# Optimization experiments

Measured on AMD Instinct MI355X. Metric: run time of the kernel, lower is better.

Reference implementation:

```python
import jax, jax.numpy as jnp
import numpy as np

HIDDEN, HEADS, HDIM = 1024, 8, 64
B, S = 4, 8192
LN_EPS = 1e-6


def setup_inputs() -> dict:
    key = jax.random.key(0)
    ks = jax.random.split(key, 12)
    inner = HEADS * HDIM
    sd = HIDDEN ** -0.5
    return {
        "x": jax.random.normal(ks[0], (B, S, HIDDEN), jnp.float32),
        "Wq": jax.random.normal(ks[1], (HIDDEN, inner), jnp.float32) * sd,
        "bq": jnp.zeros((inner,), jnp.float32),
        "Wk": jax.random.normal(ks[2], (HIDDEN, inner), jnp.float32) * sd,
        "bk": jnp.zeros((inner,), jnp.float32),
        "Wv": jax.random.normal(ks[3], (HIDDEN, inner), jnp.float32) * sd,
        "bv": jnp.zeros((inner,), jnp.float32),
        "Wo": jax.random.normal(ks[4], (inner, HIDDEN), jnp.float32) * (inner ** -0.5),
        "bo": jnp.zeros((HIDDEN,), jnp.float32),
        "alpha": jnp.ones((HEADS, HDIM), jnp.float32),
        "aug_param": jax.random.normal(ks[5], (1, HEADS, HDIM), jnp.float32),
        "ln_scale": jnp.ones((HIDDEN,), jnp.float32),
        "ln_bias": jnp.zeros((HIDDEN,), jnp.float32),
    }


def reference(x, Wq, bq, Wk, bk, Wv, bv, Wo, bo, alpha, aug_param, ln_scale, ln_bias):
    b, s, _ = x.shape
    h, d = alpha.shape
    scale = d ** -0.5
    q = (x @ Wq + bq).reshape(b, s, h, d)
    k = (x @ Wk + bk).reshape(b, s, h, d)
    v = (x @ Wv + bv).reshape(b, s, h, d)
    decay = jax.nn.sigmoid(alpha)  # (h, d)

    def step(state, qkv):
        q_t, k_t, v_t = qkv  # each (b, h, d)
        attn = jax.nn.softmax(jnp.einsum('bhd,bhd->bh', q_t, k_t) * scale, axis=-1)
        new_state = decay * state + (1.0 - decay) * attn[..., None] * v_t
        return new_state, new_state

    qs = jnp.moveaxis(q, 1, 0)  # (s, b, h, d)
    ks_ = jnp.moveaxis(k, 1, 0)
    vs = jnp.moveaxis(v, 1, 0)
    init = jnp.zeros((b, h, d), x.dtype)
    _, states = jax.lax.scan(step, init, (qs, ks_, vs))
    states = jnp.moveaxis(states, 0, 1)  # (b, s, h, d)

    aug = jax.nn.sigmoid(q * aug_param)  # aug_param (1,h,d) broadcasts over (b,s,h,d)
    out = (q * states + aug).reshape(b, s, h * d)
    out = out @ Wo + bo
    mean = jnp.mean(out, axis=-1, keepdims=True)
    var = jnp.var(out, axis=-1, keepdims=True)
    return (out - mean) * jax.lax.rsqrt(var + LN_EPS) * ln_scale + ln_bias
```

## Files before the change

### kernel.cpp

```cpp
#include <hip/hip_runtime.h>
#include <hip/hip_bf16.h>


#define HIDDEN 1024
#define HEADS 8
#define HDIM 64
#define INNER 512
#define BATCH 4
#define SEQ 8192
#define ROWS (BATCH*SEQ)
#define NCHUNK 128
#define CHLEN 64

typedef unsigned short u16;
typedef unsigned int u32;
typedef __attribute__((ext_vector_type(8))) short bf16x8;
typedef __attribute__((ext_vector_type(4))) float f32x4;

__device__ __forceinline__ float b2f(u16 u) { return __uint_as_float(((u32)u) << 16); }
__device__ __forceinline__ u16 f2b(float f) {
  u32 u = __float_as_uint(f);
  u32 r = u + 0x7fffu + ((u >> 16) & 1u);
  return (u16)(r >> 16);
}
__device__ __forceinline__ u32 pack2(float a, float b) {
  return (u32)f2b(a) | ((u32)f2b(b) << 16);
}

#define GLOAD_LDS16(gp, lp)                                                  \
  __builtin_amdgcn_global_load_lds(                                          \
      (const __attribute__((address_space(1))) u32*)(gp),                    \
      (__attribute__((address_space(3))) u32*)(lp), 16, 0, 0)

__global__ __launch_bounds__(256) void prep_x(const float* __restrict__ x,
                                              u16* __restrict__ xb) {
  size_t i = ((size_t)blockIdx.x * 256 + threadIdx.x) * 8;
  float4 a = *(const float4*)(x + i);
  float4 b = *(const float4*)(x + i + 4);
  uint4 w = {pack2(a.x, a.y), pack2(a.z, a.w), pack2(b.x, b.y), pack2(b.z, b.w)};
  *(uint4*)(xb + i) = w;
}

__global__ __launch_bounds__(256) void prep_w(
    const float* __restrict__ Wq, const float* __restrict__ Wk,
    const float* __restrict__ Wv, const float* __restrict__ Wo,
    const float* __restrict__ bq, const float* __restrict__ bk,
    const float* __restrict__ bv,
    u16* __restrict__ Wt, u16* __restrict__ Wot, float* __restrict__ bcat) {
  const int WELEM = HIDDEN * INNER;
  int idx = blockIdx.x * 256 + threadIdx.x;
  if (idx < 3 * WELEM) {
    int z = idx / WELEM;
    int rem = idx - z * WELEM;
    int n = rem >> 10;
    int k = rem & 1023;
    const float* W = (z == 0) ? Wq : (z == 1) ? Wk : Wv;
    Wt[idx] = f2b(W[k * INNER + n]);
  } else {
    int rem = idx - 3 * WELEM;
    int n = rem >> 9;
    int k = rem & 511;
    Wot[rem] = f2b(Wo[k * HIDDEN + n]);
  }
  if (idx < 3 * INNER) {
    int z = idx >> 9;
    int n = idx & 511;
    bcat[idx] = (z == 0) ? bq[n] : (z == 1) ? bk[n] : bv[n];
  }
}

template <int K, bool OUT_F32, bool SPLIT3>
__global__ __launch_bounds__(512, 2) void gemm_ring(
    const u16* __restrict__ A, const u16* __restrict__ Bt,
    const float* __restrict__ bias,
    void* __restrict__ out0, void* __restrict__ out1, void* __restrict__ out2,
    int nTilesN) {
  constexpr int NT = K / 32;
  __shared__ u16 lds[4][16384];

  const int nwg = gridDim.x;
  const int chunk = nwg >> 3;
  const int bid = blockIdx.x;
  const int lin = (bid & 7) * chunk + (bid >> 3);
  const int nt = lin % nTilesN;
  const int mt = lin / nTilesN;
  const int m0 = mt * 256, n0 = nt * 256;
  const int N = nTilesN * 256;

  const int tid = threadIdx.x;
  const int lane = tid & 63;
  const int w = tid >> 6;
  const int wm = w >> 2;
  const int wn = w & 3;
  const int r16 = lane & 15, kq = lane >> 4;

  const int rt = tid >> 2;
  const int cg = (((tid & 3) ^ (rt & 3)) << 3);
  const u16* Ag = A + (size_t)(m0 + rt) * K + cg;
  const u16* Bg = Bt + (size_t)(n0 + rt) * K + cg;
  const int ldst = w * 512;

#define STAGE(slot, kt)                                                       \
  {                                                                           \
    const u16* ga = Ag + (size_t)(kt) * 32;                                   \
    const u16* gb = Bg + (size_t)(kt) * 32;                                   \
    GLOAD_LDS16(ga, &lds[slot][ldst]);                                        \
    GLOAD_LDS16(ga + (size_t)128 * K, &lds[slot][4096 + ldst]);               \
    GLOAD_LDS16(gb, &lds[slot][8192 + ldst]);                                 \
    GLOAD_LDS16(gb + (size_t)128 * K, &lds[slot][12288 + ldst]);              \
  }

  const int xr = (r16 & 3) << 3;
  const int aO = (wm * 128 + r16) * 32 + ((kq << 3) ^ xr);
  const int bO = 8192 + (wn * 64 + r16) * 32 + ((kq << 3) ^ xr);

  f32x4 acc[8][4] = {};

#define COMPUTE(slot)                                                          \
  {                                                                            \
    const u16* sl = &lds[slot][0];                                             \
    bf16x8 af[8], bfv[4];                                                      \
    _Pragma("unroll") for (int j = 0; j < 4; j++)                              \
        bfv[j] = *(const bf16x8*)&sl[bO + j * 512];                            \
    _Pragma("unroll") for (int i = 0; i < 8; i++)                              \
        af[i] = *(const bf16x8*)&sl[aO + i * 512];                             \
    _Pragma("unroll") for (int i = 0; i < 8; i++)                              \
        _Pragma("unroll") for (int j = 0; j < 4; j++)                          \
            acc[i][j] =                                                        \
        __builtin_amdgcn_mfma_f32_16x16x32_bf16(af[i], bfv[j], acc[i][j], 0, 0, 0); \
  }

#define SYNCB                                                                  \
  {                                                                            \
    __builtin_amdgcn_sched_barrier(0);                                         \
    __builtin_amdgcn_s_barrier();                                              \
    __builtin_amdgcn_sched_barrier(0);                                         \
  }

  STAGE(0, 0);
  STAGE(1, 1);
  STAGE(2, 2);

  for (int t = 0; t < NT - 3; ++t) {
    STAGE((t + 3) & 3, t + 3);
    asm volatile("s_waitcnt vmcnt(12)" ::: "memory");
    SYNCB;
    COMPUTE(t & 3);
    SYNCB;
  }
  asm volatile("s_waitcnt vmcnt(8)" ::: "memory");
  SYNCB;
  COMPUTE((NT - 3) & 3);
  SYNCB;
  asm volatile("s_waitcnt vmcnt(4)" ::: "memory");
  SYNCB;
  COMPUTE((NT - 2) & 3);
  SYNCB;
  asm volatile("s_waitcnt vmcnt(0)" ::: "memory");
  SYNCB;
  COMPUTE((NT - 1) & 3);
#undef STAGE
#undef COMPUTE
#undef SYNCB

  const int zsel = SPLIT3 ? ((n0 + wn * 64) >> 9) : 0;
  u16* ob16 = (u16*)((zsel == 0) ? out0 : (zsel == 1) ? out1 : out2);
#pragma unroll
  for (int j = 0; j < 4; j++) {
    int col = n0 + wn * 64 + j * 16 + r16;
    float bv = bias[col];
    int colm = SPLIT3 ? (col & 511) : col;
#pragma unroll
    for (int i = 0; i < 8; i++) {
#pragma unroll
      for (int q = 0; q < 4; q++) {
        int row = m0 + wm * 128 + i * 16 + kq * 4 + q;
        float v = acc[i][j][q] + bv;
        if (OUT_F32)
          ((float*)out0)[(size_t)row * N + col] = v;
        else
          ob16[(size_t)row * INNER + colm] = f2b(v);
      }
    }
  }
}

template <bool A_BF16, bool OUT_F32>
__global__ __launch_bounds__(256) void gemm128(
    const void* __restrict__ Aany, const u16* __restrict__ BtBase,
    const float* __restrict__ bias0, const float* __restrict__ bias1,
    const float* __restrict__ bias2,
    void* __restrict__ out0, void* __restrict__ out1, void* __restrict__ out2,
    int K) {
  __shared__ u16 As[128 * 32];
  __shared__ u16 Bs[128 * 32];
  const int N = gridDim.x * 128;
  const int z = blockIdx.z;
  const u16* Bt = BtBase + (size_t)z * N * K;
  const float* bias = (z == 0) ? bias0 : (z == 1) ? bias1 : bias2;
  void* Out = (z == 0) ? out0 : (z == 1) ? out1 : out2;
  const int tid = threadIdx.x;
  const int m0 = blockIdx.y * 128;
  const int n0 = blockIdx.x * 128;
  const int lane = tid & 63;
  const int wid = tid >> 6;
  const int wm = wid >> 1, wn = wid & 1;
  const int r16 = lane & 15, kq = lane >> 4;
  const int r = tid >> 1;
  const int half = tid & 1;
  f32x4 acc[4][4] = {};
  for (int k0 = 0; k0 < K; k0 += 32) {
    __syncthreads();
    if (A_BF16) {
      const u16* Ab = (const u16*)Aany;
      const int4* src = (const int4*)(Ab + (size_t)(m0 + r) * K + k0 + half * 16);
      int4 v0 = src[0];
      int4 v1 = src[1];
      *(int4*)&As[r * 32 + half * 16] = v0;
      *(int4*)&As[r * 32 + half * 16 + 8] = v1;
    } else {
      const float* Af = (const float*)Aany;
      const float4* src = (const float4*)(Af + (size_t)(m0 + r) * K + k0 + half * 16);
      float4 f0 = src[0], f1 = src[1], f2 = src[2], f3 = src[3];
      uint4 w0 = {pack2(f0.x, f0.y), pack2(f0.z, f0.w), pack2(f1.x, f1.y), pack2(f1.z, f1.w)};
      uint4 w1 = {pack2(f2.x, f2.y), pack2(f2.z, f2.w), pack2(f3.x, f3.y), pack2(f3.z, f3.w)};
      *(uint4*)&As[r * 32 + half * 16] = w0;
      *(uint4*)&As[r * 32 + half * 16 + 8] = w1;
    }
    {
      const int4* src = (const int4*)(Bt + (size_t)(n0 + r) * K + k0 + half * 16);
      int4 v0 = src[0];
      int4 v1 = src[1];
      *(int4*)&Bs[r * 32 + half * 16] = v0;
      *(int4*)&Bs[r * 32 + half * 16 + 8] = v1;
    }
    __syncthreads();
    bf16x8 a[4], b[4];
#pragma unroll
    for (int i = 0; i < 4; i++)
      a[i] = *(const bf16x8*)&As[(wm * 64 + i * 16 + r16) * 32 + kq * 8];
#pragma unroll
    for (int j = 0; j < 4; j++)
      b[j] = *(const bf16x8*)&Bs[(wn * 64 + j * 16 + r16) * 32 + kq * 8];
#pragma unroll
    for (int i = 0; i < 4; i++)
#pragma unroll
      for (int j = 0; j < 4; j++)
        acc[i][j] = __builtin_amdgcn_mfma_f32_16x16x32_bf16(a[i], b[j], acc[i][j], 0, 0, 0);
  }
#pragma unroll
  for (int j = 0; j < 4; j++) {
    int col = n0 + wn * 64 + j * 16 + r16;
    float bv = bias[col];
#pragma unroll
    for (int i = 0; i < 4; i++) {
#pragma unroll
      for (int q = 0; q < 4; q++) {
        int row = m0 + wm * 64 + i * 16 + kq * 4 + q;
        float v = acc[i][j][q] + bv;
        if (OUT_F32)
          ((float*)Out)[(size_t)row * N + col] = v;
        else
          ((u16*)Out)[(size_t)row * N + col] = f2b(v);
      }
    }
  }
}

__global__ __launch_bounds__(256) void attn_kernel(
    const u16* __restrict__ qb, const u16* __restrict__ kb,
    float* __restrict__ attn) {
  int lane = threadIdx.x & 63;
  int wid = threadIdx.x >> 6;
  size_t t = (size_t)blockIdx.x * 4 + wid;
  int4 qv = *(const int4*)(qb + t * INNER + lane * 8);
  int4 kv = *(const int4*)(kb + t * INNER + lane * 8);
  const u16* qu = (const u16*)&qv;
  const u16* ku = (const u16*)&kv;
  float s = 0.f;
#pragma unroll
  for (int j = 0; j < 8; j++) s += b2f(qu[j]) * b2f(ku[j]);
  s += __shfl_xor(s, 1);
  s += __shfl_xor(s, 2);
  s += __shfl_xor(s, 4);
  s *= 0.125f;
  float mx = s;
  mx = fmaxf(mx, __shfl_xor(mx, 8));
  mx = fmaxf(mx, __shfl_xor(mx, 16));
  mx = fmaxf(mx, __shfl_xor(mx, 32));
  float e = __expf(s - mx);
  float sm = e;
  sm += __shfl_xor(sm, 8);
  sm += __shfl_xor(sm, 16);
  sm += __shfl_xor(sm, 32);
  float a = e / sm;
  if ((lane & 7) == 0) attn[t * HEADS + (lane >> 3)] = a;
}

__global__ __launch_bounds__(512) void scan_phase1(
    const u16* __restrict__ vb, const float* __restrict__ attn,
    const float* __restrict__ alpha, float* __restrict__ ends) {
  int hd = threadIdx.x;
  int h = hd >> 6;
  int c = blockIdx.x, b = blockIdx.y;
  float decay = 1.f / (1.f + __expf(-alpha[hd]));
  float om = 1.f - decay;
  size_t base = (size_t)b * SEQ + (size_t)c * CHLEN;
  float st = 0.f;
#pragma unroll 8
  for (int i = 0; i < CHLEN; i++) {
    size_t t = base + i;
    float a = attn[t * HEADS + h];
    float v = b2f(vb[t * INNER + hd]);
    st = decay * st + om * a * v;
  }
  ends[((size_t)b * NCHUNK + c) * INNER + hd] = st;
}

__global__ __launch_bounds__(512) void scan_phase2(
    const float* __restrict__ ends, const float* __restrict__ alpha,
    float* __restrict__ carries) {
  int hd = threadIdx.x;
  int b = blockIdx.x;
  float decay = 1.f / (1.f + __expf(-alpha[hd]));
  float dL = __powf(decay, (float)CHLEN);
  float carry = 0.f;
#pragma unroll 8
  for (int c = 0; c < NCHUNK; c++) {
    size_t idx = ((size_t)b * NCHUNK + c) * INNER + hd;
    carries[idx] = carry;
    carry = dL * carry + ends[idx];
  }
}

__global__ __launch_bounds__(512) void scan_phase3(
    const u16* __restrict__ qb, const u16* __restrict__ vb,
    const float* __restrict__ attn, const float* __restrict__ alpha,
    const float* __restrict__ augp, const float* __restrict__ carries,
    u16* __restrict__ outpre) {
  int hd = threadIdx.x;
  int h = hd >> 6;
  int c = blockIdx.x, b = blockIdx.y;
  float decay = 1.f / (1.f + __expf(-alpha[hd]));
  float om = 1.f - decay;
  float ap = augp[hd];
  float st = carries[((size_t)b * NCHUNK + c) * INNER + hd];
  size_t base = (size_t)b * SEQ + (size_t)c * CHLEN;
#pragma unroll 4
  for (int i = 0; i < CHLEN; i++) {
    size_t t = base + i;
    float a = attn[t * HEADS + h];
    float v = b2f(vb[t * INNER + hd]);
    st = decay * st + om * a * v;
    float q = b2f(qb[t * INNER + hd]);
    float aug = 1.f / (1.f + __expf(-q * ap));
    outpre[t * INNER + hd] = f2b(q * st + aug);
  }
}

__global__ __launch_bounds__(256) void ln_kernel(
    float* __restrict__ out, const float* __restrict__ lns,
    const float* __restrict__ lnb) {
  size_t row = blockIdx.x;
  int tid = threadIdx.x;
  float4 v = *(float4*)(out + row * HIDDEN + tid * 4);
  float s = v.x + v.y + v.z + v.w;
  float ss = v.x * v.x + v.y * v.y + v.z * v.z + v.w * v.w;
#pragma unroll
  for (int m = 1; m < 64; m <<= 1) {
    s += __shfl_xor(s, m);
    ss += __shfl_xor(ss, m);
  }
  __shared__ float sb[4], ssb[4];
  int lane = tid & 63, wid = tid >> 6;
  if (lane == 0) {
    sb[wid] = s;
    ssb[wid] = ss;
  }
  __syncthreads();
  s = sb[0] + sb[1] + sb[2] + sb[3];
  ss = ssb[0] + ssb[1] + ssb[2] + ssb[3];
  float mean = s * (1.f / HIDDEN);
  float var = ss * (1.f / HIDDEN) - mean * mean;
  float rstd = rsqrtf(var + 1e-6f);
  float4 sc = *(const float4*)(lns + tid * 4);
  float4 bi = *(const float4*)(lnb + tid * 4);
  v.x = (v.x - mean) * rstd * sc.x + bi.x;
  v.y = (v.y - mean) * rstd * sc.y + bi.y;
  v.z = (v.z - mean) * rstd * sc.z + bi.z;
  v.w = (v.w - mean) * rstd * sc.w + bi.w;
  *(float4*)(out + row * HIDDEN + tid * 4) = v;
}

extern "C" void kernel_launch(void* const* d_in, const int* in_sizes, int n_in,
                              void* d_out, int out_size, void* d_ws, size_t ws_size,
                              hipStream_t stream) {
  const float* x = (const float*)d_in[0];
  const float* Wq = (const float*)d_in[1];
  const float* bq = (const float*)d_in[2];
  const float* Wk = (const float*)d_in[3];
  const float* bk = (const float*)d_in[4];
  const float* Wv = (const float*)d_in[5];
  const float* bv = (const float*)d_in[6];
  const float* Wo = (const float*)d_in[7];
  const float* bo = (const float*)d_in[8];
  const float* alpha = (const float*)d_in[9];
  const float* augp = (const float*)d_in[10];
  const float* lns = (const float*)d_in[11];
  const float* lnb = (const float*)d_in[12];

  char* ws = (char*)d_ws;
  const bool fast = ws_size >= 175118336ull;

  if (fast) {
    u16* xb = (u16*)(ws + 0);
    u16* qb = (u16*)(ws + 67108864);
    u16* kb = (u16*)(ws + 100663296);
    u16* vb = (u16*)(ws + 134217728);
    u16* Wt = (u16*)(ws + 167772160);
    u16* Wot = (u16*)(ws + 170917888);
    float* bcat = (float*)(ws + 171966464);
    float* attn = (float*)(ws + 171972608);
    float* ends = (float*)(ws + 173021184);
    float* car = (float*)(ws + 174069760);
    u16* outpre = kb;

    prep_x<<<ROWS * HIDDEN / 8 / 256, 256, 0, stream>>>(x, xb);
    prep_w<<<8192, 256, 0, stream>>>(Wq, Wk, Wv, Wo, bq, bk, bv, Wt, Wot, bcat);

    gemm_ring<HIDDEN, false, true><<<768, 512, 0, stream>>>(
        xb, Wt, bcat, qb, kb, vb, 6);

    attn_kernel<<<ROWS / 4, 256, 0, stream>>>(qb, kb, attn);
    scan_phase1<<<dim3(NCHUNK, BATCH), 512, 0, stream>>>(vb, attn, alpha, ends);
    scan_phase2<<<BATCH, 512, 0, stream>>>(ends, alpha, car);
    scan_phase3<<<dim3(NCHUNK, BATCH), 512, 0, stream>>>(qb, vb, attn, alpha, augp, car, outpre);

    gemm_ring<INNER, true, false><<<512, 512, 0, stream>>>(
        outpre, Wot, bo, d_out, d_out, d_out, 4);

    ln_kernel<<<ROWS, 256, 0, stream>>>((float*)d_out, lns, lnb);
  } else {
    u16* qb = (u16*)(ws + 0);
    u16* kb = (u16*)(ws + 33554432);
    u16* vb = (u16*)(ws + 67108864);
    u16* Wt = (u16*)(ws + 100663296);
    u16* Wot = (u16*)(ws + 103809024);
    float* bcat = (float*)(ws + 104845312);
    float* attn = (float*)(ws + 104857600);
    float* ends = (float*)(ws + 105906176);
    float* car = (float*)(ws + 106954752);
    u16* outpre = kb;

    prep_w<<<8192, 256, 0, stream>>>(Wq, Wk, Wv, Wo, bq, bk, bv, Wt, Wot, bcat);
    gemm128<false, false><<<dim3(4, 256, 3), 256, 0, stream>>>(
        x, Wt, bq, bk, bv, qb, kb, vb, HIDDEN);
    attn_kernel<<<ROWS / 4, 256, 0, stream>>>(qb, kb, attn);
    scan_phase1<<<dim3(NCHUNK, BATCH), 512, 0, stream>>>(vb, attn, alpha, ends);
    scan_phase2<<<BATCH, 512, 0, stream>>>(ends, alpha, car);
    scan_phase3<<<dim3(NCHUNK, BATCH), 512, 0, stream>>>(qb, vb, attn, alpha, augp, car, outpre);
    gemm_ring<INNER, true, false><<<512, 512, 0, stream>>>(
        outpre, Wot, bo, d_out, d_out, d_out, 4);
    ln_kernel<<<ROWS, 256, 0, stream>>>((float*)d_out, lns, lnb);
  }
}
```

Baseline: 324.1 us.

## Split GEMM main loop into two phases with interleaved staging and priority hints

```diff
diff --git a/kernel.cpp b/kernel.cpp
--- a/kernel.cpp
+++ b/kernel.cpp
@@ -70,7 +70,7 @@
 }
 
 template <int K, bool OUT_F32, bool SPLIT3>
-__global__ __launch_bounds__(512, 2) void gemm_ring(
+__global__ __launch_bounds__(512, 2) void gemm_8ph(
     const u16* __restrict__ A, const u16* __restrict__ Bt,
     const float* __restrict__ bias,
     void* __restrict__ out0, void* __restrict__ out1, void* __restrict__ out2,
@@ -95,73 +95,98 @@
   const int r16 = lane & 15, kq = lane >> 4;
 
   const int rt = tid >> 2;
-  const int cg = (((tid & 3) ^ (rt & 3)) << 3);
+  const int cg = (((tid & 3) << 3)) ^ (((rt >> 1) & 3) << 3);
   const u16* Ag = A + (size_t)(m0 + rt) * K + cg;
   const u16* Bg = Bt + (size_t)(n0 + rt) * K + cg;
   const int ldst = w * 512;
 
-#define STAGE(slot, kt)                                                       \
+#define STAGE_A(slot, kt)                                                     \
   {                                                                           \
-    const u16* ga = Ag + (size_t)(kt) * 32;                                   \
-    const u16* gb = Bg + (size_t)(kt) * 32;                                   \
-    GLOAD_LDS16(ga, &lds[slot][ldst]);                                        \
-    GLOAD_LDS16(ga + (size_t)128 * K, &lds[slot][4096 + ldst]);               \
-    GLOAD_LDS16(gb, &lds[slot][8192 + ldst]);                                 \
-    GLOAD_LDS16(gb + (size_t)128 * K, &lds[slot][12288 + ldst]);              \
-  }
-
-  const int xr = (r16 & 3) << 3;
-  const int aO = (wm * 128 + r16) * 32 + ((kq << 3) ^ xr);
-  const int bO = 8192 + (wn * 64 + r16) * 32 + ((kq << 3) ^ xr);
+    GLOAD_LDS16(Ag + (size_t)(kt) * 32, &lds[slot][ldst]);                    \
+    GLOAD_LDS16(Ag + (size_t)(kt) * 32 + (size_t)128 * K,                     \
+                &lds[slot][4096 + ldst]);                                     \
+  }
+#define STAGE_B(slot, kt)                                                     \
+  {                                                                           \
+    GLOAD_LDS16(Bg + (size_t)(kt) * 32, &lds[slot][8192 + ldst]);             \
+    GLOAD_LDS16(Bg + (size_t)(kt) * 32 + (size_t)128 * K,                     \
+                &lds[slot][12288 + ldst]);                                    \
+  }
+
+  const int xk = (kq << 3) ^ (((r16 >> 1) & 3) << 3);
+  const int aO = (wm * 128 + r16) * 32 + xk;
+  const int bO = 8192 + (wn * 64 + r16) * 32 + xk;
 
   f32x4 acc[8][4] = {};
-
-#define COMPUTE(slot)                                                          \
+  bf16x8 af[4], bfv[4];
+
+#define PH0(t_, STG)                                                           \
   {                                                                            \
-    const u16* sl = &lds[slot][0];                                             \
-    bf16x8 af[8], bfv[4];                                                      \
+    const u16* sl = &lds[(t_) & 3][0];                                         \
+    _Pragma("unroll") for (int i = 0; i < 4; i++)                              \
+        af[i] = *(const bf16x8*)&sl[aO + i * 512];                             \
     _Pragma("unroll") for (int j = 0; j < 4; j++)                              \
         bfv[j] = *(const bf16x8*)&sl[bO + j * 512];                            \
-    _Pragma("unroll") for (int i = 0; i < 8; i++)                              \
-        af[i] = *(const bf16x8*)&sl[aO + i * 512];                             \
-    _Pragma("unroll") for (int i = 0; i < 8; i++)                              \
+    STG;                                                                       \
+    __builtin_amdgcn_sched_barrier(0);                                         \
+    __builtin_amdgcn_s_barrier();                                              \
+    asm volatile("s_waitcnt lgkmcnt(0)" ::: "memory");                         \
+    __builtin_amdgcn_sched_barrier(0);                                         \
+    __builtin_amdgcn_s_setprio(1);                                             \
+    _Pragma("unroll") for (int i = 0; i < 4; i++)                              \
         _Pragma("unroll") for (int j = 0; j < 4; j++)                          \
             acc[i][j] =                                                        \
         __builtin_amdgcn_mfma_f32_16x16x32_bf16(af[i], bfv[j], acc[i][j], 0, 0, 0); \
-  }
-
-#define SYNCB                                                                  \
+    __builtin_amdgcn_s_setprio(0);                                             \
+    __builtin_amdgcn_sched_barrier(0);                                         \
+    __builtin_amdgcn_s_barrier();                                              \
+  }
+
+#define PH1(t_, STG, VM)                                                       \
   {                                                                            \
+    const u16* sl = &lds[(t_) & 3][0];                                         \
+    _Pragma("unroll") for (int i = 0; i < 4; i++)                              \
+        af[i] = *(const bf16x8*)&sl[aO + (i + 4) * 512];                       \
+    STG;                                                                       \
+    asm volatile("s_waitcnt vmcnt(" #VM ")" ::: "memory");                     \
     __builtin_amdgcn_sched_barrier(0);                                         \
     __builtin_amdgcn_s_barrier();                                              \
-    __builtin_amdgcn_sched_barrier(0);                                         \
-  }
-
-  STAGE(0, 0);
-  STAGE(1, 1);
-  STAGE(2, 2);
+    asm volatile("s_waitcnt lgkmcnt(0)" ::: "memory");                         \
+    __builtin_amdgcn_sched_barrier(0);                                         \
+    __builtin_amdgcn_s_setprio(1);                                             \
+    _Pragma("unroll") for (int i = 0; i < 4; i++)                              \
+        _Pragma("unroll") for (int j = 0; j < 4; j++)                          \
+            acc[i + 4][j] =                                                    \
+        __builtin_amdgcn_mfma_f32_16x16x32_bf16(af[i], bfv[j], acc[i + 4][j], 0, 0, 0); \
+    __builtin_amdgcn_s_setprio(0);                                             \
+    __builtin_amdgcn_sched_barrier(0);                                         \
+    __builtin_amdgcn_s_barrier();                                              \
+  }
+
+#define NOSTG ((void)0)
+
+  STAGE_A(0, 0); STAGE_B(0, 0);
+  STAGE_A(1, 1); STAGE_B(1, 1);
+  STAGE_A(2, 2); STAGE_B(2, 2);
+  asm volatile("s_waitcnt vmcnt(8)" ::: "memory");
+  __builtin_amdgcn_sched_barrier(0);
+  __builtin_amdgcn_s_barrier();
 
   for (int t = 0; t < NT - 3; ++t) {
-    STAGE((t + 3) & 3, t + 3);
-    asm volatile("s_waitcnt vmcnt(12)" ::: "memory");
-    SYNCB;
-    COMPUTE(t & 3);
-    SYNCB;
-  }
-  asm volatile("s_waitcnt vmcnt(8)" ::: "memory");
-  SYNCB;
-  COMPUTE((NT - 3) & 3);
-  SYNCB;
-  asm volatile("s_waitcnt vmcnt(4)" ::: "memory");
-  SYNCB;
-  COMPUTE((NT - 2) & 3);
-  SYNCB;
-  asm volatile("s_waitcnt vmcnt(0)" ::: "memory");
-  SYNCB;
-  COMPUTE((NT - 1) & 3);
-#undef STAGE
-#undef COMPUTE
-#undef SYNCB
+    PH0(t, STAGE_A((t + 3) & 3, t + 3));
+    PH1(t, STAGE_B((t + 3) & 3, t + 3), 8);
+  }
+  PH0(NT - 3, NOSTG);
+  PH1(NT - 3, NOSTG, 4);
+  PH0(NT - 2, NOSTG);
+  PH1(NT - 2, NOSTG, 0);
+  PH0(NT - 1, NOSTG);
+  PH1(NT - 1, NOSTG, 0);
+#undef PH0
+#undef PH1
+#undef NOSTG
+#undef STAGE_A
+#undef STAGE_B
 
   const int zsel = SPLIT3 ? ((n0 + wn * 64) >> 9) : 0;
   u16* ob16 = (u16*)((zsel == 0) ? out0 : (zsel == 1) ? out1 : out2);
@@ -428,7 +453,7 @@
     prep_x<<<ROWS * HIDDEN / 8 / 256, 256, 0, stream>>>(x, xb);
     prep_w<<<8192, 256, 0, stream>>>(Wq, Wk, Wv, Wo, bq, bk, bv, Wt, Wot, bcat);
 
-    gemm_ring<HIDDEN, false, true><<<768, 512, 0, stream>>>(
+    gemm_8ph<HIDDEN, false, true><<<768, 512, 0, stream>>>(
         xb, Wt, bcat, qb, kb, vb, 6);
 
     attn_kernel<<<ROWS / 4, 256, 0, stream>>>(qb, kb, attn);
@@ -436,7 +461,7 @@
     scan_phase2<<<BATCH, 512, 0, stream>>>(ends, alpha, car);
     scan_phase3<<<dim3(NCHUNK, BATCH), 512, 0, stream>>>(qb, vb, attn, alpha, augp, car, outpre);
 
-    gemm_ring<INNER, true, false><<<512, 512, 0, stream>>>(
+    gemm_8ph<INNER, true, false><<<512, 512, 0, stream>>>(
         outpre, Wot, bo, d_out, d_out, d_out, 4);
 
     ln_kernel<<<ROWS, 256, 0, stream>>>((float*)d_out, lns, lnb);
@@ -459,7 +484,7 @@
     scan_phase1<<<dim3(NCHUNK, BATCH), 512, 0, stream>>>(vb, attn, alpha, ends);
     scan_phase2<<<BATCH, 512, 0, stream>>>(ends, alpha, car);
     scan_phase3<<<dim3(NCHUNK, BATCH), 512, 0, stream>>>(qb, vb, attn, alpha, augp, car, outpre);
-    gemm_ring<INNER, true, false><<<512, 512, 0, stream>>>(
+    gemm_8ph<INNER, true, false><<<512, 512, 0, stream>>>(
         outpre, Wot, bo, d_out, d_out, d_out, 4);
     ln_kernel<<<ROWS, 256, 0, stream>>>((float*)d_out, lns, lnb);
   }
```

Measured after the change: 320.3 us. About the same (-1.2%).
